# Kernel tuning notes

Measured on AMD Instinct MI355X. Metric: run time of the kernel, lower is better.

Reference implementation:

```python
import jax, jax.numpy as jnp
import numpy as np

N_NODES = 50000
N_EDGES = 800000
D_FEAT = 64


def setup_inputs() -> dict:
    key = jax.random.key(0)
    k1, k2, k3, k4, k5 = jax.random.split(key, 5)
    features = jax.random.normal(k1, (N_NODES, D_FEAT), dtype=jnp.float32)
    src_idx = jax.random.randint(k2, (N_EDGES,), 0, N_NODES, dtype=jnp.int64)
    dst_idx = jax.random.randint(k3, (N_EDGES,), 0, N_NODES, dtype=jnp.int64)
    # MLP params: Linear(64,64) -> ReLU -> Linear(64,1) -> ReLU
    W1 = jax.random.normal(k4, (D_FEAT, D_FEAT), dtype=jnp.float32) * (1.0 / np.sqrt(D_FEAT))
    b1 = jnp.zeros((D_FEAT,), dtype=jnp.float32)
    W2 = jax.random.normal(k5, (D_FEAT, 1), dtype=jnp.float32) * (1.0 / np.sqrt(D_FEAT))
    b2 = jnp.zeros((1,), dtype=jnp.float32)
    return {"features": features, "src_idx": src_idx, "dst_idx": dst_idx,
            "W1": W1, "b1": b1, "W2": W2, "b2": b2}


def reference(features, src_idx, dst_idx, W1, b1, W2, b2):
    src_f = features[src_idx]            # [E, D]
    dst_f = features[dst_idx]            # [E, D]
    dif = src_f - dst_f                  # [E, D]
    h = jax.nn.relu(dif @ W1 + b1)       # [E, D]
    att = jax.nn.relu(h @ W2 + b2)       # [E, 1]
    att = jnp.exp(-att)                  # [E, 1]
    feature = att * dst_f                # [E, D]
    return feature
```

## Files before the change

### kernel.cpp

```cpp
#include <hip/hip_runtime.h>
#include <hip/hip_bf16.h>
#include <math.h>


#define D 64
#define NPB 64

__global__ __launch_bounds__(256) void node_proj_kernel(
    const float* __restrict__ F, const float* __restrict__ W1,
    float* __restrict__ P, int n_nodes)
{
    __shared__ float sW[D * D];
    __shared__ float sF[NPB * D];

    const int tid = threadIdx.x;
    const int base = blockIdx.x * NPB;
    const int nrows = min(NPB, n_nodes - base);

    const float4* W4 = (const float4*)W1;
    float4* sW4 = (float4*)sW;
#pragma unroll
    for (int i = 0; i < 4; ++i) sW4[tid + i * 256] = W4[tid + i * 256];

    const float4* F4 = (const float4*)(F + (long)base * D);
    float4* sF4 = (float4*)sF;
    const int totalf4 = nrows * (D / 4);
    for (int i = tid; i < totalf4; i += 256) sF4[i] = F4[i];
    __syncthreads();

    const int col = tid & 63;
    const int q = tid >> 6;

    float acc[16];
#pragma unroll
    for (int i = 0; i < 16; ++i) acc[i] = 0.f;

    for (int k = 0; k < D; ++k) {
        const float w = sW[k * D + col];
#pragma unroll
        for (int i = 0; i < 16; ++i)
            acc[i] += sF[(q + i * 4) * D + k] * w;
    }

#pragma unroll
    for (int i = 0; i < 16; ++i) {
        const int n = q + i * 4;
        if (n < nrows) P[(long)(base + n) * D + col] = acc[i];
    }
}

__global__ __launch_bounds__(256) void edge_kernel(
    const float* __restrict__ P, const float* __restrict__ F,
    const int* __restrict__ src_idx, const int* __restrict__ dst_idx,
    const float* __restrict__ b1, const float* __restrict__ W2,
    const float* __restrict__ b2v,
    float* __restrict__ out, int n_edges)
{
    const int tid = blockIdx.x * blockDim.x + threadIdx.x;
    const int lane16 = threadIdx.x & 15;
    const int e = tid >> 4;
    if (e >= n_edges) return;

    const float4 b1f = ((const float4*)b1)[lane16];
    const float4 w2f = ((const float4*)W2)[lane16];
    const float b2s = b2v[0];

    const long s = (long)src_idx[e];
    const long d = (long)dst_idx[e];

    const float4 ps = ((const float4*)P)[s * 16 + lane16];
    const float4 pd = ((const float4*)P)[d * 16 + lane16];
    const float4 fd = ((const float4*)F)[d * 16 + lane16];

    float hx = fmaxf(ps.x - pd.x + b1f.x, 0.f);
    float hy = fmaxf(ps.y - pd.y + b1f.y, 0.f);
    float hz = fmaxf(ps.z - pd.z + b1f.z, 0.f);
    float hw = fmaxf(ps.w - pd.w + b1f.w, 0.f);

    float dot = hx * w2f.x + hy * w2f.y + hz * w2f.z + hw * w2f.w;
    dot += __shfl_xor(dot, 1);
    dot += __shfl_xor(dot, 2);
    dot += __shfl_xor(dot, 4);
    dot += __shfl_xor(dot, 8);

    const float att = fmaxf(dot + b2s, 0.f);
    const float a = __expf(-att);

    float4 o;
    o.x = a * fd.x; o.y = a * fd.y; o.z = a * fd.z; o.w = a * fd.w;
    ((float4*)out)[(long)e * 16 + lane16] = o;
}

extern "C" void kernel_launch(void* const* d_in, const int* in_sizes, int n_in,
                              void* d_out, int out_size, void* d_ws, size_t ws_size,
                              hipStream_t stream) {
    const float* features = (const float*)d_in[0];
    const int*   src_idx  = (const int*)d_in[1];
    const int*   dst_idx  = (const int*)d_in[2];
    const float* W1       = (const float*)d_in[3];
    const float* b1       = (const float*)d_in[4];
    const float* W2       = (const float*)d_in[5];
    const float* b2       = (const float*)d_in[6];
    float* out = (float*)d_out;

    const int n_nodes = in_sizes[0] / D;
    const int n_edges = in_sizes[1];

    float* P = (float*)d_ws;

    const int grid1 = (n_nodes + NPB - 1) / NPB;
    node_proj_kernel<<<grid1, 256, 0, stream>>>(features, W1, P, n_nodes);

    const int groups_per_block = 256 / 16;
    const int grid2 = (n_edges + groups_per_block - 1) / groups_per_block;
    edge_kernel<<<grid2, 256, 0, stream>>>(P, features, src_idx, dst_idx,
                                           b1, W2, b2, out, n_edges);
}
```

Baseline: 299.7 us.

## Batch edge gathers per thread, use nontemporal output stores, register-tile node projection

Each 16-lane group in the edge kernel now handles four edges strided by the grid size. All index loads and row gathers are issued before any compute, giving more memory-level parallelism per thread. Output rows are written with nontemporal stores so the large streaming output does not evict the gathered feature and projection rows from cache. The node projection is rewritten as a 4x4 register-tiled float4 matmul that reads shared memory as float4. The cost is higher register pressure and a quarter as many edge blocks.

```diff
diff --git a/kernel.cpp b/kernel.cpp
--- a/kernel.cpp
+++ b/kernel.cpp
@@ -5,90 +5,114 @@
 
 #define D 64
 #define NPB 64
+#define U 4
+
+typedef float nfloat4 __attribute__((ext_vector_type(4)));
 
 __global__ __launch_bounds__(256) void node_proj_kernel(
     const float* __restrict__ F, const float* __restrict__ W1,
     float* __restrict__ P, int n_nodes)
 {
-    __shared__ float sW[D * D];
-    __shared__ float sF[NPB * D];
+    __shared__ float4 sW4[D * 16];
+    __shared__ float4 sF4[NPB * 16];
 
     const int tid = threadIdx.x;
     const int base = blockIdx.x * NPB;
     const int nrows = min(NPB, n_nodes - base);
 
     const float4* W4 = (const float4*)W1;
-    float4* sW4 = (float4*)sW;
 #pragma unroll
     for (int i = 0; i < 4; ++i) sW4[tid + i * 256] = W4[tid + i * 256];
 
-    const float4* F4 = (const float4*)(F + (long)base * D);
-    float4* sF4 = (float4*)sF;
-    const int totalf4 = nrows * (D / 4);
-    for (int i = tid; i < totalf4; i += 256) sF4[i] = F4[i];
+    const float4* Fg = (const float4*)(F + (long)base * D);
+    const int totalf4 = nrows * 16;
+    for (int i = tid; i < totalf4; i += 256) sF4[i] = Fg[i];
     __syncthreads();
 
-    const int col = tid & 63;
-    const int q = tid >> 6;
+    const int tx = tid & 15;
+    const int ty = tid >> 4;
 
-    float acc[16];
+    float4 acc[4];
 #pragma unroll
-    for (int i = 0; i < 16; ++i) acc[i] = 0.f;
+    for (int i = 0; i < 4; ++i) { acc[i].x = 0.f; acc[i].y = 0.f; acc[i].z = 0.f; acc[i].w = 0.f; }
 
-    for (int k = 0; k < D; ++k) {
-        const float w = sW[k * D + col];
 #pragma unroll
-        for (int i = 0; i < 16; ++i)
-            acc[i] += sF[(q + i * 4) * D + k] * w;
+    for (int k4 = 0; k4 < 16; ++k4) {
+        float4 wr[4], fr[4];
+#pragma unroll
+        for (int r = 0; r < 4; ++r) wr[r] = sW4[(k4 * 4 + r) * 16 + tx];
+#pragma unroll
+        for (int i = 0; i < 4; ++i) fr[i] = sF4[(ty * 4 + i) * 16 + k4];
+#pragma unroll
+        for (int i = 0; i < 4; ++i) {
+            acc[i].x += fr[i].x * wr[0].x + fr[i].y * wr[1].x + fr[i].z * wr[2].x + fr[i].w * wr[3].x;
+            acc[i].y += fr[i].x * wr[0].y + fr[i].y * wr[1].y + fr[i].z * wr[2].y + fr[i].w * wr[3].y;
+            acc[i].z += fr[i].x * wr[0].z + fr[i].y * wr[1].z + fr[i].z * wr[2].z + fr[i].w * wr[3].z;
+            acc[i].w += fr[i].x * wr[0].w + fr[i].y * wr[1].w + fr[i].z * wr[2].w + fr[i].w * wr[3].w;
+        }
     }
 
 #pragma unroll
-    for (int i = 0; i < 16; ++i) {
-        const int n = q + i * 4;
-        if (n < nrows) P[(long)(base + n) * D + col] = acc[i];
+    for (int i = 0; i < 4; ++i) {
+        const int n = ty * 4 + i;
+        if (n < nrows) ((float4*)P)[(long)(base + n) * 16 + tx] = acc[i];
     }
 }
 
-__global__ __launch_bounds__(256) void edge_kernel(
-    const float* __restrict__ P, const float* __restrict__ F,
+__global__ __launch_bounds__(256, 4) void edge_kernel(
+    const float4* __restrict__ P4, const float4* __restrict__ F4,
     const int* __restrict__ src_idx, const int* __restrict__ dst_idx,
     const float* __restrict__ b1, const float* __restrict__ W2,
     const float* __restrict__ b2v,
-    float* __restrict__ out, int n_edges)
+    float4* __restrict__ out4, int n_edges, int G)
 {
-    const int tid = blockIdx.x * blockDim.x + threadIdx.x;
     const int lane16 = threadIdx.x & 15;
-    const int e = tid >> 4;
-    if (e >= n_edges) return;
+    const int g = (blockIdx.x * blockDim.x + threadIdx.x) >> 4;
 
     const float4 b1f = ((const float4*)b1)[lane16];
     const float4 w2f = ((const float4*)W2)[lane16];
     const float b2s = b2v[0];
 
-    const long s = (long)src_idx[e];
-    const long d = (long)dst_idx[e];
+    int e[U]; bool ok[U]; long s[U], d[U];
+#pragma unroll
+    for (int j = 0; j < U; ++j) {
+        e[j] = g + j * G;
+        ok[j] = e[j] < n_edges;
+        const int ee = ok[j] ? e[j] : 0;
+        s[j] = (long)src_idx[ee];
+        d[j] = (long)dst_idx[ee];
+    }
 
-    const float4 ps = ((const float4*)P)[s * 16 + lane16];
-    const float4 pd = ((const float4*)P)[d * 16 + lane16];
-    const float4 fd = ((const float4*)F)[d * 16 + lane16];
+    float4 ps[U], pd[U], fd[U];
+#pragma unroll
+    for (int j = 0; j < U; ++j) {
+        ps[j] = P4[s[j] * 16 + lane16];
+        pd[j] = P4[d[j] * 16 + lane16];
+        fd[j] = F4[d[j] * 16 + lane16];
+    }
 
-    float hx = fmaxf(ps.x - pd.x + b1f.x, 0.f);
-    float hy = fmaxf(ps.y - pd.y + b1f.y, 0.f);
-    float hz = fmaxf(ps.z - pd.z + b1f.z, 0.f);
-    float hw = fmaxf(ps.w - pd.w + b1f.w, 0.f);
+#pragma unroll
+    for (int j = 0; j < U; ++j) {
+        const float hx = fmaxf(ps[j].x - pd[j].x + b1f.x, 0.f);
+        const float hy = fmaxf(ps[j].y - pd[j].y + b1f.y, 0.f);
+        const float hz = fmaxf(ps[j].z - pd[j].z + b1f.z, 0.f);
+        const float hw = fmaxf(ps[j].w - pd[j].w + b1f.w, 0.f);
 
-    float dot = hx * w2f.x + hy * w2f.y + hz * w2f.z + hw * w2f.w;
-    dot += __shfl_xor(dot, 1);
-    dot += __shfl_xor(dot, 2);
-    dot += __shfl_xor(dot, 4);
-    dot += __shfl_xor(dot, 8);
+        float dot = hx * w2f.x + hy * w2f.y + hz * w2f.z + hw * w2f.w;
+        dot += __shfl_xor(dot, 1);
+        dot += __shfl_xor(dot, 2);
+        dot += __shfl_xor(dot, 4);
+        dot += __shfl_xor(dot, 8);
 
-    const float att = fmaxf(dot + b2s, 0.f);
-    const float a = __expf(-att);
+        const float a = __expf(-fmaxf(dot + b2s, 0.f));
 
-    float4 o;
-    o.x = a * fd.x; o.y = a * fd.y; o.z = a * fd.z; o.w = a * fd.w;
-    ((float4*)out)[(long)e * 16 + lane16] = o;
+        nfloat4 o;
+        o.x = a * fd[j].x; o.y = a * fd[j].y; o.z = a * fd[j].z; o.w = a * fd[j].w;
+        if (ok[j]) {
+            nfloat4* dst = (nfloat4*)&out4[(long)e[j] * 16 + lane16];
+            __builtin_nontemporal_store(o, dst);
+        }
+    }
 }
 
 extern "C" void kernel_launch(void* const* d_in, const int* in_sizes, int n_in,
@@ -111,8 +135,9 @@
     const int grid1 = (n_nodes + NPB - 1) / NPB;
     node_proj_kernel<<<grid1, 256, 0, stream>>>(features, W1, P, n_nodes);
 
-    const int groups_per_block = 256 / 16;
-    const int grid2 = (n_edges + groups_per_block - 1) / groups_per_block;
-    edge_kernel<<<grid2, 256, 0, stream>>>(P, features, src_idx, dst_idx,
-                                           b1, W2, b2, out, n_edges);
+    const int grid2 = (n_edges + 16 * U - 1) / (16 * U);
+    const int G = grid2 * 16;
+    edge_kernel<<<grid2, 256, 0, stream>>>((const float4*)P, (const float4*)features,
+                                           src_idx, dst_idx, b1, W2, b2,
+                                           (float4*)out, n_edges, G);
 }
```

Result: slower. 322.7 us (+7.7%).
